# Kernel optimization log

Measured on AMD Instinct MI355X. Metric: run time of the kernel, lower is better.

## Reference

```python
import jax, jax.numpy as jnp
import numpy as np

NB_HEAD = 16
SIZE_PER_HEAD = 64
D_MODEL = NB_HEAD * SIZE_PER_HEAD  # 1024
B, L = 2, 2048
NEG_BIG = 1e12


def setup_inputs() -> dict:
    key = jax.random.key(0)
    ks = jax.random.split(key, 8)
    return {
        "Q_seq": jax.random.normal(ks[0], (B, L, D_MODEL), dtype=jnp.float32),
        "K_seq": jax.random.normal(ks[1], (B, L, D_MODEL), dtype=jnp.float32),
        "V_seq": jax.random.normal(ks[2], (B, L, D_MODEL), dtype=jnp.float32),
        "q_len": jax.random.randint(ks[3], (B, 1), 1, L, dtype=jnp.int32),
        "v_len": jax.random.randint(ks[4], (B, 1), 1, L, dtype=jnp.int32),
        "WQ": jax.random.normal(ks[5], (D_MODEL, D_MODEL), dtype=jnp.float32) * 0.02,
        "WK": jax.random.normal(ks[6], (D_MODEL, D_MODEL), dtype=jnp.float32) * 0.02,
        "WV": jax.random.normal(ks[7], (D_MODEL, D_MODEL), dtype=jnp.float32) * 0.02,
    }


def _len_mask(lens, length, dtype):
    # Keras code: mask = 1 - cumsum(one_hot(len, L)) -> 1 for pos < len, 0 otherwise
    return (jnp.arange(length)[None, :] < lens).astype(dtype)  # [B, L]


def reference(Q_seq, K_seq, V_seq, q_len, v_len, WQ, WK, WV):
    Bq, Lq, _ = Q_seq.shape
    Lk = K_seq.shape[1]
    # QKV projections, split heads: [B, H, L, D]
    q = (Q_seq @ WQ).reshape(Bq, Lq, NB_HEAD, SIZE_PER_HEAD).transpose(0, 2, 1, 3)
    k = (K_seq @ WK).reshape(Bq, Lk, NB_HEAD, SIZE_PER_HEAD).transpose(0, 2, 1, 3)
    v = (V_seq @ WV).reshape(Bq, Lk, NB_HEAD, SIZE_PER_HEAD).transpose(0, 2, 1, 3)
    # scaled dot-product scores [B, H, Lq, Lk]
    scores = jnp.einsum("bhqd,bhkd->bhqk", q, k) / np.float32(SIZE_PER_HEAD ** 0.5)
    # additive key-length mask (V_len), matching Mask(..., 'add')
    kmask = _len_mask(v_len, Lk, scores.dtype)  # [B, Lk]
    scores = scores - (1.0 - kmask)[:, None, None, :] * np.float32(NEG_BIG)
    A = jax.nn.softmax(scores, axis=-1)
    # attention output, merge heads: [B, Lq, H*D]
    O = jnp.einsum("bhqk,bhkd->bqhd", A, v).reshape(Bq, Lq, D_MODEL)
    # multiplicative query-length mask (Q_len), matching Mask(..., 'mul')
    qmask = _len_mask(q_len, Lq, O.dtype)  # [B, Lq]
    return O * qmask[:, :, None]
```

## Files before the change

### kernel.cpp

```cpp
#include <hip/hip_runtime.h>
#include <cstddef>

#define NB_HEAD 16
#define HEAD_DIM 64
#define D_MODEL 1024
#define BATCH 2
#define SEQ 2048
#define MROWS (BATCH * SEQ)

typedef __bf16 bf16x8 __attribute__((ext_vector_type(8)));
typedef __bf16 bf16x4 __attribute__((ext_vector_type(4)));
typedef float  f32x4  __attribute__((ext_vector_type(4)));

#define XEL ((size_t)MROWS * D_MODEL)
#define WEL ((size_t)D_MODEL * D_MODEL)

static __device__ __forceinline__ size_t xchunk(int row, int k) {
    return ((size_t)(row >> 4) * 32 + (k >> 5)) * 512 + ((k >> 3) & 3) * 128 + (row & 15) * 8 + (k & 7);
}
static __device__ __forceinline__ size_t qkbase(int bh, int row16, int dc) {
    return ((size_t)(bh * 128 + row16) * 2 + dc) * 512;
}
static __device__ __forceinline__ size_t qkelem(int bh, int row, int d) {
    return qkbase(bh, row >> 4, d >> 5) + ((d >> 3) & 3) * 128 + (row & 15) * 8 + (d & 7);
}
static __device__ __forceinline__ size_t vbase(int bh, int d16, int kc) {
    return ((size_t)(bh * 4 + d16) * 64 + kc) * 512;
}
static __device__ __forceinline__ size_t velem(int bh, int d, int key) {
    return vbase(bh, d >> 4, key >> 5) + ((key >> 3) & 3) * 128 + (d & 15) * 8 + (key & 7);
}

static __device__ __forceinline__ void split_bf16(float x, __bf16& h, __bf16& l) {
    h = (__bf16)x;
    l = (__bf16)(x - (float)h);
}

__global__ __launch_bounds__(256) void conv_wt_kernel(
    const float* __restrict__ W0, const float* __restrict__ W1,
    const float* __restrict__ W2,
    __bf16* __restrict__ hi, __bf16* __restrict__ lo)
{
    __shared__ float tile[64][65];
    const int t  = threadIdx.x;
    const int k0 = blockIdx.x * 64;
    const int n0 = blockIdx.y * 64;
    const int z  = blockIdx.z;
    const float* W = (z == 0) ? W0 : ((z == 1) ? W1 : W2);
    __bf16* hz = hi + (size_t)z * WEL;
    __bf16* lz = lo + (size_t)z * WEL;

    #pragma unroll
    for (int p = 0; p < 4; ++p) {
        const int e = (p * 256 + t) * 4;
        const int r = e >> 6, c = e & 63;
        const float4 v = *(const float4*)(W + (size_t)(k0 + r) * D_MODEL + n0 + c);
        tile[r][c] = v.x; tile[r][c + 1] = v.y; tile[r][c + 2] = v.z; tile[r][c + 3] = v.w;
    }
    __syncthreads();
    #pragma unroll
    for (int p = 0; p < 4; ++p) {
        const int e = (p * 256 + t) * 4;
        const int n = e >> 6, kc = e & 63;
        __bf16 h[4], l[4];
        #pragma unroll
        for (int u = 0; u < 4; ++u) split_bf16(tile[kc + u][n], h[u], l[u]);
        const size_t a = xchunk(n0 + n, k0 + kc);
        *(bf16x4*)(hz + a) = (bf16x4){h[0], h[1], h[2], h[3]};
        *(bf16x4*)(lz + a) = (bf16x4){l[0], l[1], l[2], l[3]};
    }
}

__global__ __launch_bounds__(256) void conv_x_kernel(
    const float* __restrict__ X0, const float* __restrict__ X1,
    const float* __restrict__ X2,
    const int* __restrict__ q_len, const int* __restrict__ v_len,
    __bf16* __restrict__ xhi, __bf16* __restrict__ xlo)
{
    const int z = blockIdx.y;
    const size_t e = ((size_t)blockIdx.x * 256 + threadIdx.x) * 8;
    const int l = (int)(e >> 10), k = (int)(e & 1023);
    const int bb = l >> 11, lb = l & (SEQ - 1);
    const int len = (z == 0) ? q_len[bb] : v_len[bb];
    if (lb >= ((len + 127) & ~127)) return;

    const float* X = (z == 0) ? X0 : ((z == 1) ? X1 : X2);
    const float4 v0 = *(const float4*)(X + e);
    const float4 v1 = *(const float4*)(X + e + 4);
    const float xs[8] = {v0.x, v0.y, v0.z, v0.w, v1.x, v1.y, v1.z, v1.w};
    bf16x8 h8, l8;
    #pragma unroll
    for (int u = 0; u < 8; ++u) { __bf16 h_, l_; split_bf16(xs[u], h_, l_); h8[u] = h_; l8[u] = l_; }
    const size_t a = z * XEL + xchunk(l, k);
    *(bf16x8*)(xhi + a) = h8;
    *(bf16x8*)(xlo + a) = l8;
}

__global__ __launch_bounds__(256, 2) void proj_mfma_kernel(
    const __bf16* __restrict__ Xhi, const __bf16* __restrict__ Xlo,
    const __bf16* __restrict__ Wchi, const __bf16* __restrict__ Wclo,
    const int* __restrict__ q_len, const int* __restrict__ v_len,
    __bf16* __restrict__ qch, __bf16* __restrict__ qcl,
    __bf16* __restrict__ kch, __bf16* __restrict__ kcl,
    __bf16* __restrict__ vch, __bf16* __restrict__ vcl)
{
    const int t    = threadIdx.x;
    const int wave = t >> 6, lane = t & 63;
    const int li   = lane & 15, grp = lane >> 4;
    const int wm   = wave >> 1, wn = wave & 1;
    const int m0   = blockIdx.x * 128;
    const int n0   = blockIdx.y * 128;
    const int z    = blockIdx.z;
    const int bb   = m0 >> 11;
    const int l0   = m0 & (SEQ - 1);
    const int need = (z == 0) ? q_len[bb] : v_len[bb];
    if (l0 >= need) return;

    const __bf16* Xh = Xhi + z * XEL;
    const __bf16* Xl = Xlo + z * XEL;
    const __bf16* Wh = Wchi + z * WEL;
    const __bf16* Wl = Wclo + z * WEL;

    const size_t abase = ((size_t)((m0 >> 4) + wm * 4) * 32) * 512 + lane * 8;
    const size_t bbase = ((size_t)((n0 >> 4) + wn * 4) * 32) * 512 + lane * 8;

    f32x4 acc[4][4] = {};
    bf16x8 ah[2][4], al[2][4], bh[2][4], bl[2][4];

    #pragma unroll
    for (int i = 0; i < 4; ++i) {
        ah[0][i] = *(const bf16x8*)(Xh + abase + (size_t)i * 16384);
        al[0][i] = *(const bf16x8*)(Xl + abase + (size_t)i * 16384);
        bh[0][i] = *(const bf16x8*)(Wh + bbase + (size_t)i * 16384);
        bl[0][i] = *(const bf16x8*)(Wl + bbase + (size_t)i * 16384);
    }

    #pragma unroll 2
    for (int kc = 0; kc < 32; ++kc) {
        const int cur = kc & 1, nxt = cur ^ 1;
        if (kc < 31) {
            const size_t ka = abase + (size_t)(kc + 1) * 512;
            const size_t kb = bbase + (size_t)(kc + 1) * 512;
            #pragma unroll
            for (int i = 0; i < 4; ++i) {
                ah[nxt][i] = *(const bf16x8*)(Xh + ka + (size_t)i * 16384);
                al[nxt][i] = *(const bf16x8*)(Xl + ka + (size_t)i * 16384);
                bh[nxt][i] = *(const bf16x8*)(Wh + kb + (size_t)i * 16384);
                bl[nxt][i] = *(const bf16x8*)(Wl + kb + (size_t)i * 16384);
            }
        }
        #pragma unroll
        for (int j = 0; j < 4; ++j) {
            #pragma unroll
            for (int i = 0; i < 4; ++i) {
                acc[i][j] = __builtin_amdgcn_mfma_f32_16x16x32_bf16(ah[cur][i], bh[cur][j], acc[i][j], 0, 0, 0);
                acc[i][j] = __builtin_amdgcn_mfma_f32_16x16x32_bf16(ah[cur][i], bl[cur][j], acc[i][j], 0, 0, 0);
                acc[i][j] = __builtin_amdgcn_mfma_f32_16x16x32_bf16(al[cur][i], bh[cur][j], acc[i][j], 0, 0, 0);
            }
        }
    }

    #pragma unroll
    for (int j = 0; j < 4; ++j) {
        const int cg = n0 + wn * 64 + j * 16 + li;
        const int hd = cg >> 6, d = cg & 63;
        const int bhI = bb * NB_HEAD + hd;
        #pragma unroll
        for (int i = 0; i < 4; ++i) {
            #pragma unroll
            for (int r = 0; r < 4; ++r) {
                const int rg = m0 + wm * 64 + i * 16 + grp * 4 + r;
                const int lg = rg & (SEQ - 1);
                __bf16 h_, l_;
                split_bf16(acc[i][j][r], h_, l_);
                if (z == 0) {
                    const size_t a = qkelem(bhI, lg, d);
                    qch[a] = h_; qcl[a] = l_;
                } else if (z == 1) {
                    const size_t a = qkelem(bhI, lg, d);
                    kch[a] = h_; kcl[a] = l_;
                } else {
                    const size_t a = velem(bhI, d, lg);
                    vch[a] = h_; vcl[a] = l_;
                }
            }
        }
    }
}

__global__ __launch_bounds__(256, 2) void attn_mfma_kernel(
    const __bf16* __restrict__ qch, const __bf16* __restrict__ qcl,
    const __bf16* __restrict__ kch, const __bf16* __restrict__ kcl,
    const __bf16* __restrict__ vch, const __bf16* __restrict__ vcl,
    const int* __restrict__ q_len, const int* __restrict__ v_len,
    float* __restrict__ out)
{
    __shared__ __align__(16) __bf16 Ps[128][72];

    const int t = threadIdx.x;
    const int wq = t >> 6, lane = t & 63;
    const int grp = lane >> 4, li = lane & 15;
    const int hh = blockIdx.x;
    const int q0 = blockIdx.y * 128;
    const int b  = blockIdx.z;
    const int qlen = q_len[b], vlen = v_len[b];
    const int bh = b * NB_HEAD + hh;
    const int qbase = q0 + wq * 32;

    if (qbase >= qlen) {
        const int row = qbase + (lane >> 1), cs = (lane & 1) * 32;
        float* o = out + ((size_t)b * SEQ + row) * D_MODEL + hh * HEAD_DIM + cs;
        const float4 z4 = make_float4(0.f, 0.f, 0.f, 0.f);
        #pragma unroll
        for (int u = 0; u < 8; ++u) *(float4*)(o + u * 4) = z4;
        return;
    }

    bf16x8 qh[2][2], ql[2][2];
    #pragma unroll
    for (int s = 0; s < 2; ++s)
        #pragma unroll
        for (int ks = 0; ks < 2; ++ks) {
            const size_t a = qkbase(bh, (qbase >> 4) + s, ks) + lane * 8;
            qh[s][ks] = *(const bf16x8*)(qch + a);
            ql[s][ks] = *(const bf16x8*)(qcl + a);
        }

    f32x4 O[2][4] = {};
    float m_s[2][4], l_s[2][4];
    #pragma unroll
    for (int s = 0; s < 2; ++s)
        #pragma unroll
        for (int r = 0; r < 4; ++r) { m_s[s][r] = -1e30f; l_s[s][r] = 0.f; }

    const int nkt = (vlen + 63) >> 6;

    for (int tt = 0; tt < nkt; ++tt) {
        const int k0 = tt * 64;

        f32x4 sacc[2][4] = {};
        #pragma unroll
        for (int ks = 0; ks < 2; ++ks) {
            bf16x8 kh_[4], kl_[4];
            #pragma unroll
            for (int j = 0; j < 4; ++j) {
                const size_t a = qkbase(bh, (k0 >> 4) + j, ks) + lane * 8;
                kh_[j] = *(const bf16x8*)(kch + a);
                kl_[j] = *(const bf16x8*)(kcl + a);
            }
            #pragma unroll
            for (int j = 0; j < 4; ++j)
                #pragma unroll
                for (int s = 0; s < 2; ++s) {
                    sacc[s][j] = __builtin_amdgcn_mfma_f32_16x16x32_bf16(qh[s][ks], kh_[j], sacc[s][j], 0, 0, 0);
                    sacc[s][j] = __builtin_amdgcn_mfma_f32_16x16x32_bf16(qh[s][ks], kl_[j], sacc[s][j], 0, 0, 0);
                    sacc[s][j] = __builtin_amdgcn_mfma_f32_16x16x32_bf16(ql[s][ks], kh_[j], sacc[s][j], 0, 0, 0);
                }
        }

        bf16x8 vh_[2][4], vl_[2][4];
        #pragma unroll
        for (int ks = 0; ks < 2; ++ks)
            #pragma unroll
            for (int j = 0; j < 4; ++j) {
                const size_t a = vbase(bh, j, (k0 >> 5) + ks) + lane * 8;
                vh_[ks][j] = *(const bf16x8*)(vch + a);
                vl_[ks][j] = *(const bf16x8*)(vcl + a);
            }

        #pragma unroll
        for (int s = 0; s < 2; ++s) {
            float mx[4] = {-1e30f, -1e30f, -1e30f, -1e30f};
            #pragma unroll
            for (int j = 0; j < 4; ++j) {
                const int key = k0 + j * 16 + li;
                #pragma unroll
                for (int r = 0; r < 4; ++r) {
                    float v = sacc[s][j][r] * 0.125f;
                    if (key >= vlen) v = -1e30f;
                    sacc[s][j][r] = v;
                    mx[r] = fmaxf(mx[r], v);
                }
            }
            #pragma unroll
            for (int r = 0; r < 4; ++r) {
                mx[r] = fmaxf(mx[r], __shfl_xor(mx[r], 1));
                mx[r] = fmaxf(mx[r], __shfl_xor(mx[r], 2));
                mx[r] = fmaxf(mx[r], __shfl_xor(mx[r], 4));
                mx[r] = fmaxf(mx[r], __shfl_xor(mx[r], 8));
            }
            float al[4], sum[4];
            #pragma unroll
            for (int r = 0; r < 4; ++r) {
                const float mn = fmaxf(m_s[s][r], mx[r]);
                al[r] = __expf(m_s[s][r] - mn);
                m_s[s][r] = mn;
                sum[r] = 0.f;
            }
            #pragma unroll
            for (int j = 0; j < 4; ++j)
                #pragma unroll
                for (int r = 0; r < 4; ++r) {
                    const float p = __expf(sacc[s][j][r] - m_s[s][r]);
                    const __bf16 pb = (__bf16)p;
                    sum[r] += (float)pb;
                    Ps[wq * 32 + s * 16 + grp * 4 + r][j * 16 + li] = pb;
                }
            #pragma unroll
            for (int r = 0; r < 4; ++r) {
                sum[r] += __shfl_xor(sum[r], 1);
                sum[r] += __shfl_xor(sum[r], 2);
                sum[r] += __shfl_xor(sum[r], 4);
                sum[r] += __shfl_xor(sum[r], 8);
                l_s[s][r] = l_s[s][r] * al[r] + sum[r];
            }
            #pragma unroll
            for (int j = 0; j < 4; ++j)
                #pragma unroll
                for (int r = 0; r < 4; ++r) O[s][j][r] *= al[r];
        }
        asm volatile("s_waitcnt lgkmcnt(0)" ::: "memory");

        #pragma unroll
        for (int ks = 0; ks < 2; ++ks) {
            bf16x8 pa[2];
            #pragma unroll
            for (int s = 0; s < 2; ++s)
                pa[s] = *(const bf16x8*)&Ps[wq * 32 + s * 16 + li][ks * 32 + grp * 8];
            #pragma unroll
            for (int j = 0; j < 4; ++j)
                #pragma unroll
                for (int s = 0; s < 2; ++s) {
                    O[s][j] = __builtin_amdgcn_mfma_f32_16x16x32_bf16(pa[s], vh_[ks][j], O[s][j], 0, 0, 0);
                    O[s][j] = __builtin_amdgcn_mfma_f32_16x16x32_bf16(pa[s], vl_[ks][j], O[s][j], 0, 0, 0);
                }
        }
    }

    #pragma unroll
    for (int s = 0; s < 2; ++s)
        #pragma unroll
        for (int r = 0; r < 4; ++r) {
            const int q = qbase + s * 16 + grp * 4 + r;
            const float inv = (q < qlen) ? 1.f / l_s[s][r] : 0.f;
            #pragma unroll
            for (int j = 0; j < 4; ++j)
                out[((size_t)b * SEQ + q) * D_MODEL + hh * HEAD_DIM + j * 16 + li] = O[s][j][r] * inv;
        }
}

extern "C" void kernel_launch(void* const* d_in, const int* in_sizes, int n_in,
                              void* d_out, int out_size, void* d_ws, size_t ws_size,
                              hipStream_t stream)
{
    (void)in_sizes; (void)n_in; (void)out_size; (void)ws_size;
    const float* Q_seq = (const float*)d_in[0];
    const float* K_seq = (const float*)d_in[1];
    const float* V_seq = (const float*)d_in[2];
    const int*   q_len = (const int*)d_in[3];
    const int*   v_len = (const int*)d_in[4];
    const float* WQ    = (const float*)d_in[5];
    const float* WK    = (const float*)d_in[6];
    const float* WV    = (const float*)d_in[7];
    float* out = (float*)d_out;

    __bf16* wchi = (__bf16*)d_ws;
    __bf16* wclo = wchi + 3 * WEL;
    __bf16* xhi_ = wclo + 3 * WEL;
    __bf16* xlo_ = xhi_ + 3 * XEL;
    __bf16* qch_ = xlo_ + 3 * XEL;
    __bf16* qcl_ = qch_ + XEL;
    __bf16* kch_ = qcl_ + XEL;
    __bf16* kcl_ = kch_ + XEL;
    __bf16* vch_ = kcl_ + XEL;
    __bf16* vcl_ = vch_ + XEL;

    dim3 blk(256);

    dim3 cg(D_MODEL / 64, D_MODEL / 64, 3);
    conv_wt_kernel<<<cg, blk, 0, stream>>>(WQ, WK, WV, wchi, wclo);

    dim3 xg((unsigned)(XEL / 2048), 3);
    conv_x_kernel<<<xg, blk, 0, stream>>>(Q_seq, K_seq, V_seq, q_len, v_len, xhi_, xlo_);

    dim3 pg(MROWS / 128, D_MODEL / 128, 3);
    proj_mfma_kernel<<<pg, blk, 0, stream>>>(xhi_, xlo_, wchi, wclo, q_len, v_len,
                                             qch_, qcl_, kch_, kcl_, vch_, vcl_);

    dim3 ag(NB_HEAD, SEQ / 128, BATCH);
    attn_mfma_kernel<<<ag, blk, 0, stream>>>(qch_, qcl_, kch_, kcl_, vch_, vcl_,
                                             q_len, v_len, out);
}
```

Measured before the change: 305.7 us.

## Stage projection GEMM operands through LDS with async global-to-LDS loads

The projection GEMM now loads its A and B tiles into double-buffered shared memory using global_load_lds, one wave per operand (X hi/lo, W hi/lo). Before, each wave loaded its own fragments straight from global memory into registers, so every tile was fetched twice by the two waves that share it. Sharing tiles through LDS halves the global traffic and frees registers. In exchange it adds a block-wide barrier every k-step and uses 64 KB of LDS, which may limit occupancy.

```diff
diff --git a/kernel.cpp b/kernel.cpp
--- a/kernel.cpp
+++ b/kernel.cpp
@@ -34,6 +34,12 @@
 static __device__ __forceinline__ void split_bf16(float x, __bf16& h, __bf16& l) {
     h = (__bf16)x;
     l = (__bf16)(x - (float)h);
+}
+
+static __device__ __forceinline__ void gload_lds16(const __bf16* g, __bf16* l) {
+    __builtin_amdgcn_global_load_lds((const __attribute__((address_space(1))) void*)g,
+                                     (__attribute__((address_space(3))) void*)l,
+                                     16, 0, 0);
 }
 
 __global__ __launch_bounds__(256) void conv_wt_kernel(
@@ -104,6 +110,8 @@
     __bf16* __restrict__ kch, __bf16* __restrict__ kcl,
     __bf16* __restrict__ vch, __bf16* __restrict__ vcl)
 {
+    __shared__ __align__(16) __bf16 lds[2][2][2][8][512];
+
     const int t    = threadIdx.x;
     const int wave = t >> 6, lane = t & 63;
     const int li   = lane & 15, grp = lane >> 4;
@@ -121,43 +129,45 @@
     const __bf16* Wh = Wchi + z * WEL;
     const __bf16* Wl = Wclo + z * WEL;
 
-    const size_t abase = ((size_t)((m0 >> 4) + wm * 4) * 32) * 512 + lane * 8;
-    const size_t bbase = ((size_t)((n0 >> 4) + wn * 4) * 32) * 512 + lane * 8;
+    const __bf16* gsrc = (wave == 0) ? Xh : (wave == 1) ? Xl : (wave == 2) ? Wh : Wl;
+    const size_t  cb16 = (size_t)((wave < 2) ? (m0 >> 4) : (n0 >> 4));
+
+    auto STAGE = [&](int buf, int kc) {
+        #pragma unroll
+        for (int u = 0; u < 8; ++u) {
+            const __bf16* g = gsrc + ((cb16 + (size_t)u) * 32 + (size_t)kc) * 512 + (size_t)lane * 8;
+            gload_lds16(g, &lds[buf][wm][wn][u][0]);
+        }
+    };
 
     f32x4 acc[4][4] = {};
-    bf16x8 ah[2][4], al[2][4], bh[2][4], bl[2][4];
-
-    #pragma unroll
-    for (int i = 0; i < 4; ++i) {
-        ah[0][i] = *(const bf16x8*)(Xh + abase + (size_t)i * 16384);
-        al[0][i] = *(const bf16x8*)(Xl + abase + (size_t)i * 16384);
-        bh[0][i] = *(const bf16x8*)(Wh + bbase + (size_t)i * 16384);
-        bl[0][i] = *(const bf16x8*)(Wl + bbase + (size_t)i * 16384);
-    }
+
+    STAGE(0, 0);
+    __syncthreads();
 
     #pragma unroll 2
     for (int kc = 0; kc < 32; ++kc) {
-        const int cur = kc & 1, nxt = cur ^ 1;
-        if (kc < 31) {
-            const size_t ka = abase + (size_t)(kc + 1) * 512;
-            const size_t kb = bbase + (size_t)(kc + 1) * 512;
+        const int cur = kc & 1;
+        if (kc < 31) STAGE(cur ^ 1, kc + 1);
+
+        bf16x8 ah[4], al4[4], bh4[4], bl4[4];
+        #pragma unroll
+        for (int i = 0; i < 4; ++i) {
+            ah[i]  = *(const bf16x8*)&lds[cur][0][0][(wm << 2) + i][lane * 8];
+            al4[i] = *(const bf16x8*)&lds[cur][0][1][(wm << 2) + i][lane * 8];
+            bh4[i] = *(const bf16x8*)&lds[cur][1][0][(wn << 2) + i][lane * 8];
+            bl4[i] = *(const bf16x8*)&lds[cur][1][1][(wn << 2) + i][lane * 8];
+        }
+        #pragma unroll
+        for (int j = 0; j < 4; ++j) {
             #pragma unroll
             for (int i = 0; i < 4; ++i) {
-                ah[nxt][i] = *(const bf16x8*)(Xh + ka + (size_t)i * 16384);
-                al[nxt][i] = *(const bf16x8*)(Xl + ka + (size_t)i * 16384);
-                bh[nxt][i] = *(const bf16x8*)(Wh + kb + (size_t)i * 16384);
-                bl[nxt][i] = *(const bf16x8*)(Wl + kb + (size_t)i * 16384);
-            }
-        }
-        #pragma unroll
-        for (int j = 0; j < 4; ++j) {
-            #pragma unroll
-            for (int i = 0; i < 4; ++i) {
-                acc[i][j] = __builtin_amdgcn_mfma_f32_16x16x32_bf16(ah[cur][i], bh[cur][j], acc[i][j], 0, 0, 0);
-                acc[i][j] = __builtin_amdgcn_mfma_f32_16x16x32_bf16(ah[cur][i], bl[cur][j], acc[i][j], 0, 0, 0);
-                acc[i][j] = __builtin_amdgcn_mfma_f32_16x16x32_bf16(al[cur][i], bh[cur][j], acc[i][j], 0, 0, 0);
-            }
-        }
+                acc[i][j] = __builtin_amdgcn_mfma_f32_16x16x32_bf16(ah[i],  bh4[j], acc[i][j], 0, 0, 0);
+                acc[i][j] = __builtin_amdgcn_mfma_f32_16x16x32_bf16(ah[i],  bl4[j], acc[i][j], 0, 0, 0);
+                acc[i][j] = __builtin_amdgcn_mfma_f32_16x16x32_bf16(al4[i], bh4[j], acc[i][j], 0, 0, 0);
+            }
+        }
+        __syncthreads();
     }
 
     #pragma unroll
```

New measurement: 284.4 us. 1.07x faster.
